# Kernel tuning notes

Measured on AMD Instinct MI355X. Metric: run time of the kernel, lower is better.

## Reference

```python
import jax, jax.numpy as jnp
import numpy as np

E, T, D, N_RBF, N_SBF = 262144, 1048576, 128, 6, 42


def setup_inputs() -> dict:
    key = jax.random.key(0)
    ks = jax.random.split(key, 24)
    s = 0.05
    inp = {
        "m_ji": jax.random.normal(ks[0], (E, D), jnp.float32),
        "e_rbf": jax.random.normal(ks[1], (E, N_RBF), jnp.float32),
        "a_sbf": jax.random.normal(ks[2], (T, N_SBF), jnp.float32),
        "nbr_list": jax.random.randint(ks[3], (E, 2), 0, 65536),
        "kj_idx": jax.random.randint(ks[4], (T,), 0, E),
        "ji_idx": jax.random.randint(ks[5], (T,), 0, E),
        # edge branch params
        "We": jax.random.normal(ks[6], (N_RBF, D), jnp.float32) * s,
        "W_e1": jax.random.normal(ks[7], (D, D), jnp.float32) * s,
        "b_e1": jnp.zeros((D,), jnp.float32),
        "W_e2": jax.random.normal(ks[8], (D, D), jnp.float32) * s,
        "b_e2": jnp.zeros((D,), jnp.float32),
        "W_e3": jax.random.normal(ks[9], (D, D), jnp.float32) * s,
        "b_e3": jnp.zeros((D,), jnp.float32),
        "W_e4": jax.random.normal(ks[10], (D, D), jnp.float32) * s,
        # angle branch params
        "Wa": jax.random.normal(ks[11], (N_SBF, D), jnp.float32) * s,
        "W_a1": jax.random.normal(ks[12], (D, D), jnp.float32) * s,
        "b_a1": jnp.zeros((D,), jnp.float32),
        "W_a2": jax.random.normal(ks[13], (D, D), jnp.float32) * s,
        "b_a2": jnp.zeros((D,), jnp.float32),
        "W_a3": jax.random.normal(ks[14], (D, D), jnp.float32) * s,
        "b_a3": jnp.zeros((D,), jnp.float32),
        "W_a4": jax.random.normal(ks[15], (D, D), jnp.float32) * s,
    }
    return inp


def _mlp(x, W1, b1, W2, b2, W3, b3, W4):
    x = jax.nn.silu(x @ W1 + b1)
    x = jax.nn.silu(x @ W2 + b2)
    x = jax.nn.silu(x @ W3 + b3)
    return x @ W4


def reference(m_ji, e_rbf, a_sbf, nbr_list, kj_idx, ji_idx,
              We, W_e1, b_e1, W_e2, b_e2, W_e3, b_e3, W_e4,
              Wa, W_a1, b_a1, W_a2, b_a2, W_a3, b_a3, W_a4):
    # edge branch: project rbf to embed dim, gate by edge messages  [E, D]
    edge_feats = _mlp((e_rbf @ We) * m_ji, W_e1, b_e1, W_e2, b_e2, W_e3, b_e3, W_e4)
    # angle branch: project sbf, gate by triplet-gathered message sum  [T, D]
    angle_gate = m_ji[kj_idx] + m_ji[ji_idx]
    angle_feats = _mlp((a_sbf @ Wa) * angle_gate, W_a1, b_a1, W_a2, b_a2, W_a3, b_a3, W_a4)
    return (edge_feats, angle_feats)
```

## Files before the change

kernel.cpp:

```cpp
#include <hip/hip_runtime.h>
#include <stdint.h>

typedef __attribute__((ext_vector_type(8))) short bf16x8;
typedef __attribute__((ext_vector_type(4))) float f32x4;
typedef __attribute__((ext_vector_type(8))) unsigned short us8;
typedef __bf16 bf16v2 __attribute__((ext_vector_type(2)));

#define T_CNT 1048576
#define E_CNT 262144

static __device__ __forceinline__ unsigned short f2bf_u(float f) {
  __bf16 h = (__bf16)f;
  return __builtin_bit_cast(unsigned short, h);
}
static __device__ __forceinline__ uint32_t pack2bf(float a, float b) {
  bf16v2 t; t[0] = (__bf16)a; t[1] = (__bf16)b;
  return __builtin_bit_cast(uint32_t, t);
}
static __device__ __forceinline__ float silu_f(float v) {
  float e = __builtin_amdgcn_exp2f(v * -1.44269504088896341f);
  return v * __builtin_amdgcn_rcpf(1.0f + e);
}
static __device__ __forceinline__ bf16x8 frag8(f32x4 a, f32x4 b) {
  union { bf16x8 v; uint32_t u[4]; } r;
  r.u[0] = pack2bf(a[0], a[1]); r.u[1] = pack2bf(a[2], a[3]);
  r.u[2] = pack2bf(b[0], b[1]); r.u[3] = pack2bf(b[2], b[3]);
  return r.v;
}

template<bool LAST>
static __device__ __forceinline__ void layer_mfma(
    const char* __restrict__ src, char* __restrict__ dst,
    const char* __restrict__ wbase,
    const float* __restrict__ bias,
    float* __restrict__ gout,
    int l15, int q, int w, int rs)
{
  f32x4 acc[2][4];
  #pragma unroll
  for (int rg = 0; rg < 2; ++rg)
    #pragma unroll
    for (int c = 0; c < 4; ++c) { f32x4 z = {0.f,0.f,0.f,0.f}; acc[rg][c] = z; }

  const int lane16 = (l15 | (q << 4)) * 16;
  #pragma unroll
  for (int ks = 0; ks < 4; ++ks) {
    bf16x8 wf[4];
    #pragma unroll
    for (int c = 0; c < 4; ++c)
      wf[c] = *(const bf16x8*)(wbase + (((w * 4 + c) * 4 + ks) << 10) + lane16);
    bf16x8 xf0 = *(const bf16x8*)(src + ((l15 * 256 + ks * 64 + q * 16) ^ rs));
    bf16x8 xf1 = *(const bf16x8*)(src + (((16 + l15) * 256 + ks * 64 + q * 16) ^ rs));
    #pragma unroll
    for (int c = 0; c < 4; ++c) {
      acc[0][c] = __builtin_amdgcn_mfma_f32_16x16x32_bf16(wf[c], xf0, acc[0][c], 0, 0, 0);
      acc[1][c] = __builtin_amdgcn_mfma_f32_16x16x32_bf16(wf[c], xf1, acc[1][c], 0, 0, 0);
    }
  }

  #pragma unroll
  for (int rg = 0; rg < 2; ++rg) {
    const int row = rg * 16 + l15;
    #pragma unroll
    for (int c = 0; c < 4; ++c) {
      if (!LAST) {
        f32x4 bv = *(const f32x4*)(bias + w * 64 + c * 16 + q * 4);
        uint2 u;
        u.x = pack2bf(silu_f(acc[rg][c][0] + bv[0]), silu_f(acc[rg][c][1] + bv[1]));
        u.y = pack2bf(silu_f(acc[rg][c][2] + bv[2]), silu_f(acc[rg][c][3] + bv[3]));
        *(uint2*)(dst + ((row * 256 + w * 128 + c * 32 + q * 8) ^ rs)) = u;
      } else {
        __builtin_nontemporal_store(acc[rg][c],
            (f32x4*)(gout + (size_t)row * 128 + w * 64 + c * 16 + q * 4));
      }
    }
  }
}

__global__ __launch_bounds__(128)
__attribute__((amdgpu_waves_per_eu(4, 5)))
void angle_kernel(
    const float* __restrict__ m_ji, const float* __restrict__ a_sbf,
    const int* __restrict__ kj, const int* __restrict__ ji,
    const float* __restrict__ b1, const float* __restrict__ b2,
    const float* __restrict__ b3,
    const char* __restrict__ wt4, const char* __restrict__ waT,
    float* __restrict__ out)
{
  __shared__ __align__(16) char xbA[8192];
  __shared__ __align__(16) char xbB[8192];
  const int tid = threadIdx.x, lane = tid & 63, w = tid >> 6;
  const int l15 = lane & 15, q = lane >> 4;
  const int rs = (l15 & 7) << 4;
  const size_t tb = (size_t)blockIdx.x * 32;
  const int lane16 = lane * 16;

  #pragma unroll
  for (int rg = 0; rg < 2; ++rg) {
    const int row = rg * 16 + l15;
    const size_t grow = tb + row;
    const int ikj = kj[grow], iji = ji[grow];
    const float* ap = a_sbf + grow * 42;
    f32x4 a0 = *(const f32x4*)(ap + q * 8);
    f32x4 a1 = *(const f32x4*)(ap + q * 8 + 4);
    f32x4 c0 = {0.f,0.f,0.f,0.f}, c1 = {0.f,0.f,0.f,0.f};
    if (q == 0) { c0 = *(const f32x4*)(ap + 32); c1 = *(const f32x4*)(ap + 36); }
    else if (q == 1) { float2 t = *(const float2*)(ap + 40); c0[0] = t.x; c0[1] = t.y; }
    bf16x8 f0 = frag8(a0, a1);
    bf16x8 f1 = frag8(c0, c1);
    #pragma unroll
    for (int c = 0; c < 4; ++c) {
      const int ct = w * 4 + c;
      bf16x8 wa0 = *(const bf16x8*)(waT + ((ct * 2 + 0) << 10) + lane16);
      bf16x8 wa1 = *(const bf16x8*)(waT + ((ct * 2 + 1) << 10) + lane16);
      f32x4 acc = {0.f,0.f,0.f,0.f};
      acc = __builtin_amdgcn_mfma_f32_16x16x32_bf16(wa0, f0, acc, 0, 0, 0);
      acc = __builtin_amdgcn_mfma_f32_16x16x32_bf16(wa1, f1, acc, 0, 0, 0);
      const float* bk = m_ji + (size_t)ikj * 128 + ct * 16 + q * 4;
      const float* bj = m_ji + (size_t)iji * 128 + ct * 16 + q * 4;
      f32x4 pk = *(const f32x4*)(bk);
      f32x4 pj = *(const f32x4*)(bj);
      f32x4 g = pk + pj;
      uint2 u;
      u.x = pack2bf(acc[0] * g[0], acc[1] * g[1]);
      u.y = pack2bf(acc[2] * g[2], acc[3] * g[3]);
      *(uint2*)(xbA + ((row * 256 + w * 128 + c * 32 + q * 8) ^ rs)) = u;
    }
  }
  __syncthreads();

  layer_mfma<false>(xbA, xbB, wt4,           b1, nullptr, l15, q, w, rs);
  __syncthreads();
  layer_mfma<false>(xbB, xbA, wt4 + 32768,   b2, nullptr, l15, q, w, rs);
  __syncthreads();
  layer_mfma<false>(xbA, xbB, wt4 + 65536,   b3, nullptr, l15, q, w, rs);
  __syncthreads();
  layer_mfma<true >(xbB, nullptr, wt4 + 98304, nullptr,
                    out + tb * 128, l15, q, w, rs);
}

__global__ __launch_bounds__(128)
__attribute__((amdgpu_waves_per_eu(4, 5)))
void edge_kernel(
    const float* __restrict__ m_ji, const float* __restrict__ e_rbf,
    const float* __restrict__ b1, const float* __restrict__ b2,
    const float* __restrict__ b3,
    const char* __restrict__ wt4, const char* __restrict__ weT,
    float* __restrict__ out)
{
  __shared__ __align__(16) char xbA[8192];
  __shared__ __align__(16) char xbB[8192];
  const int tid = threadIdx.x, lane = tid & 63, w = tid >> 6;
  const int l15 = lane & 15, q = lane >> 4;
  const int rs = (l15 & 7) << 4;
  const size_t tb = (size_t)blockIdx.x * 32;
  const int lane16 = lane * 16;

  #pragma unroll
  for (int rg = 0; rg < 2; ++rg) {
    const int row = rg * 16 + l15;
    const size_t grow = tb + row;
    const float* ep = e_rbf + grow * 6;
    f32x4 a0 = {0.f,0.f,0.f,0.f}, a1 = {0.f,0.f,0.f,0.f};
    if (q == 0) {
      a0 = *(const f32x4*)(ep);
      float2 t = *(const float2*)(ep + 4);
      a1[0] = t.x; a1[1] = t.y;
    }
    bf16x8 ef = frag8(a0, a1);
    #pragma unroll
    for (int c = 0; c < 4; ++c) {
      const int ct = w * 4 + c;
      bf16x8 we = *(const bf16x8*)(weT + (ct << 10) + lane16);
      f32x4 acc = {0.f,0.f,0.f,0.f};
      acc = __builtin_amdgcn_mfma_f32_16x16x32_bf16(we, ef, acc, 0, 0, 0);
      f32x4 g = *(const f32x4*)(m_ji + grow * 128 + ct * 16 + q * 4);
      uint2 u;
      u.x = pack2bf(acc[0] * g[0], acc[1] * g[1]);
      u.y = pack2bf(acc[2] * g[2], acc[3] * g[3]);
      *(uint2*)(xbA + ((row * 256 + w * 128 + c * 32 + q * 8) ^ rs)) = u;
    }
  }
  __syncthreads();

  layer_mfma<false>(xbA, xbB, wt4,           b1, nullptr, l15, q, w, rs);
  __syncthreads();
  layer_mfma<false>(xbB, xbA, wt4 + 32768,   b2, nullptr, l15, q, w, rs);
  __syncthreads();
  layer_mfma<false>(xbA, xbB, wt4 + 65536,   b3, nullptr, l15, q, w, rs);
  __syncthreads();
  layer_mfma<true >(xbB, nullptr, wt4 + 98304, nullptr,
                    out + tb * 128, l15, q, w, rs);
}

__global__ void prep_kernel(
    const float* __restrict__ W0, const float* __restrict__ W1,
    const float* __restrict__ W2, const float* __restrict__ W3,
    const float* __restrict__ W4, const float* __restrict__ W5,
    const float* __restrict__ W6, const float* __restrict__ W7,
    const float* __restrict__ Wa, const float* __restrict__ We,
    char* __restrict__ ws)
{
  const int gid = blockIdx.x * 256 + threadIdx.x;
  const int lane = gid & 63;
  const int l15 = lane & 15, q = lane >> 4;
  if (gid < 16384) {
    const int mat = gid >> 11;
    const int ctks = (gid & 2047) >> 6;
    const int n = (ctks >> 2) * 16 + l15;
    const int k0 = (ctks & 3) * 32 + q * 8;
    const float* W;
    switch (mat) {
      case 0: W = W0; break; case 1: W = W1; break;
      case 2: W = W2; break; case 3: W = W3; break;
      case 4: W = W4; break; case 5: W = W5; break;
      case 6: W = W6; break; default: W = W7; break;
    }
    us8 v;
    #pragma unroll
    for (int j = 0; j < 8; ++j) v[j] = f2bf_u(W[(size_t)(k0 + j) * 128 + n]);
    *(us8*)(ws + mat * 32768 + ctks * 1024 + lane * 16) = v;
  } else if (gid < 17408) {
    const int g = gid - 16384;
    const int ctks = g >> 6;
    const int n = (ctks >> 1) * 16 + l15;
    const int k0 = (ctks & 1) * 32 + q * 8;
    us8 v;
    #pragma unroll
    for (int j = 0; j < 8; ++j) {
      const int k = k0 + j;
      v[j] = (k < 42) ? f2bf_u(Wa[(size_t)k * 128 + n]) : (unsigned short)0;
    }
    *(us8*)(ws + 262144 + ctks * 1024 + lane * 16) = v;
  } else if (gid < 17920) {
    const int g = gid - 17408;
    const int ct = g >> 6;
    const int n = ct * 16 + l15;
    const int k0 = q * 8;
    us8 v;
    #pragma unroll
    for (int j = 0; j < 8; ++j) {
      const int k = k0 + j;
      v[j] = (k < 6) ? f2bf_u(We[(size_t)k * 128 + n]) : (unsigned short)0;
    }
    *(us8*)(ws + 278528 + ct * 1024 + lane * 16) = v;
  }
}

extern "C" void kernel_launch(void* const* d_in, const int* in_sizes, int n_in,
                              void* d_out, int out_size, void* d_ws, size_t ws_size,
                              hipStream_t stream) {
  (void)in_sizes; (void)n_in; (void)out_size; (void)ws_size;
  const float* m_ji  = (const float*)d_in[0];
  const float* e_rbf = (const float*)d_in[1];
  const float* a_sbf = (const float*)d_in[2];
  const int*   kj    = (const int*)d_in[4];
  const int*   ji    = (const int*)d_in[5];
  const float* We    = (const float*)d_in[6];
  const float* We1   = (const float*)d_in[7];
  const float* be1   = (const float*)d_in[8];
  const float* We2   = (const float*)d_in[9];
  const float* be2   = (const float*)d_in[10];
  const float* We3   = (const float*)d_in[11];
  const float* be3   = (const float*)d_in[12];
  const float* We4   = (const float*)d_in[13];
  const float* Wa    = (const float*)d_in[14];
  const float* Wa1   = (const float*)d_in[15];
  const float* ba1   = (const float*)d_in[16];
  const float* Wa2   = (const float*)d_in[17];
  const float* ba2   = (const float*)d_in[18];
  const float* Wa3   = (const float*)d_in[19];
  const float* ba3   = (const float*)d_in[20];
  const float* Wa4   = (const float*)d_in[21];
  char* ws = (char*)d_ws;
  float* out = (float*)d_out;

  prep_kernel<<<70, 256, 0, stream>>>(
      We1, We2, We3, We4, Wa1, Wa2, Wa3, Wa4, Wa, We, ws);
  edge_kernel<<<E_CNT / 32, 128, 0, stream>>>(
      m_ji, e_rbf, be1, be2, be3, ws, ws + 278528, out);
  angle_kernel<<<T_CNT / 32, 128, 0, stream>>>(
      m_ji, a_sbf, kj, ji, ba1, ba2, ba3, ws + 131072, ws + 262144,
      out + (size_t)E_CNT * 128);
}
```

Measured before the change: 580.0 us.

## Restructure MLP kernels to 64-row tiles with 4 waves and lean loops

Blocks grow from 32 rows and 2 waves to 64 rows and 4 waves, each wave owning 32 output columns. The four dense layers become a rolled loop that keeps only one accumulator live and reuses each weight fragment across four row groups. The gather of m_ji is hoisted ahead of the sbf/rbf projection. The aim is lower register pressure, higher occupancy and less repeated weight loading, at the cost of more LDS per block, loops that are no longer unrolled, and dependent MFMA chains on a single accumulator.

```diff
diff --git a/kernel.cpp b/kernel.cpp
--- a/kernel.cpp
+++ b/kernel.cpp
@@ -28,58 +28,81 @@
   return r.v;
 }
 
-template<bool LAST>
-static __device__ __forceinline__ void layer_mfma(
-    const char* __restrict__ src, char* __restrict__ dst,
-    const char* __restrict__ wbase,
-    const float* __restrict__ bias,
-    float* __restrict__ gout,
+static __device__ __forceinline__ void mlp4_lean(
+    char* __restrict__ xbA, char* __restrict__ xbB,
+    const char* __restrict__ wt4,
+    const float* __restrict__ b1, const float* __restrict__ b2,
+    const float* __restrict__ b3, float* __restrict__ outT,
     int l15, int q, int w, int rs)
 {
-  f32x4 acc[2][4];
-  #pragma unroll
-  for (int rg = 0; rg < 2; ++rg)
-    #pragma unroll
-    for (int c = 0; c < 4; ++c) { f32x4 z = {0.f,0.f,0.f,0.f}; acc[rg][c] = z; }
-
+  const int cb = w * 32;
   const int lane16 = (l15 | (q << 4)) * 16;
-  #pragma unroll
-  for (int ks = 0; ks < 4; ++ks) {
-    bf16x8 wf[4];
-    #pragma unroll
-    for (int c = 0; c < 4; ++c)
-      wf[c] = *(const bf16x8*)(wbase + (((w * 4 + c) * 4 + ks) << 10) + lane16);
-    bf16x8 xf0 = *(const bf16x8*)(src + ((l15 * 256 + ks * 64 + q * 16) ^ rs));
-    bf16x8 xf1 = *(const bf16x8*)(src + (((16 + l15) * 256 + ks * 64 + q * 16) ^ rs));
-    #pragma unroll
-    for (int c = 0; c < 4; ++c) {
-      acc[0][c] = __builtin_amdgcn_mfma_f32_16x16x32_bf16(wf[c], xf0, acc[0][c], 0, 0, 0);
-      acc[1][c] = __builtin_amdgcn_mfma_f32_16x16x32_bf16(wf[c], xf1, acc[1][c], 0, 0, 0);
-    }
-  }
-
-  #pragma unroll
-  for (int rg = 0; rg < 2; ++rg) {
-    const int row = rg * 16 + l15;
-    #pragma unroll
-    for (int c = 0; c < 4; ++c) {
-      if (!LAST) {
-        f32x4 bv = *(const f32x4*)(bias + w * 64 + c * 16 + q * 4);
+  const char* src = xbA;
+  char* dst = xbB;
+
+  #pragma unroll 1
+  for (int L = 0; L < 3; ++L) {
+    const char* wb = wt4 + (L << 15);
+    const float* bp = (L == 0) ? b1 : (L == 1) ? b2 : b3;
+    #pragma unroll 1
+    for (int ct = 0; ct < 2; ++ct) {
+      const char* wcb = wb + (((w * 2 + ct) * 4) << 10);
+      bf16x8 wf0 = *(const bf16x8*)(wcb + lane16);
+      bf16x8 wf1 = *(const bf16x8*)(wcb + 1024 + lane16);
+      bf16x8 wf2 = *(const bf16x8*)(wcb + 2048 + lane16);
+      bf16x8 wf3 = *(const bf16x8*)(wcb + 3072 + lane16);
+      f32x4 bv = *(const f32x4*)(bp + cb + ct * 16 + q * 4);
+      #pragma unroll
+      for (int rg = 0; rg < 4; ++rg) {
+        const int row = rg * 16 + l15;
+        bf16x8 xf0 = *(const bf16x8*)(src + ((row * 256 + q * 16) ^ rs));
+        bf16x8 xf1 = *(const bf16x8*)(src + ((row * 256 + 64 + q * 16) ^ rs));
+        bf16x8 xf2 = *(const bf16x8*)(src + ((row * 256 + 128 + q * 16) ^ rs));
+        bf16x8 xf3 = *(const bf16x8*)(src + ((row * 256 + 192 + q * 16) ^ rs));
+        f32x4 acc = {0.f,0.f,0.f,0.f};
+        acc = __builtin_amdgcn_mfma_f32_16x16x32_bf16(wf0, xf0, acc, 0, 0, 0);
+        acc = __builtin_amdgcn_mfma_f32_16x16x32_bf16(wf1, xf1, acc, 0, 0, 0);
+        acc = __builtin_amdgcn_mfma_f32_16x16x32_bf16(wf2, xf2, acc, 0, 0, 0);
+        acc = __builtin_amdgcn_mfma_f32_16x16x32_bf16(wf3, xf3, acc, 0, 0, 0);
         uint2 u;
-        u.x = pack2bf(silu_f(acc[rg][c][0] + bv[0]), silu_f(acc[rg][c][1] + bv[1]));
-        u.y = pack2bf(silu_f(acc[rg][c][2] + bv[2]), silu_f(acc[rg][c][3] + bv[3]));
-        *(uint2*)(dst + ((row * 256 + w * 128 + c * 32 + q * 8) ^ rs)) = u;
-      } else {
-        __builtin_nontemporal_store(acc[rg][c],
-            (f32x4*)(gout + (size_t)row * 128 + w * 64 + c * 16 + q * 4));
+        u.x = pack2bf(silu_f(acc[0] + bv[0]), silu_f(acc[1] + bv[1]));
+        u.y = pack2bf(silu_f(acc[2] + bv[2]), silu_f(acc[3] + bv[3]));
+        *(uint2*)(dst + ((row * 256 + cb * 2 + ct * 32 + q * 8) ^ rs)) = u;
       }
     }
-  }
-}
-
-__global__ __launch_bounds__(128)
-__attribute__((amdgpu_waves_per_eu(4, 5)))
-void angle_kernel(
+    __syncthreads();
+    const char* t = src; src = dst; dst = (char*)t;
+  }
+
+  {
+    const char* wb = wt4 + (3 << 15);
+    #pragma unroll 1
+    for (int ct = 0; ct < 2; ++ct) {
+      const char* wcb = wb + (((w * 2 + ct) * 4) << 10);
+      bf16x8 wf0 = *(const bf16x8*)(wcb + lane16);
+      bf16x8 wf1 = *(const bf16x8*)(wcb + 1024 + lane16);
+      bf16x8 wf2 = *(const bf16x8*)(wcb + 2048 + lane16);
+      bf16x8 wf3 = *(const bf16x8*)(wcb + 3072 + lane16);
+      #pragma unroll
+      for (int rg = 0; rg < 4; ++rg) {
+        const int row = rg * 16 + l15;
+        bf16x8 xf0 = *(const bf16x8*)(src + ((row * 256 + q * 16) ^ rs));
+        bf16x8 xf1 = *(const bf16x8*)(src + ((row * 256 + 64 + q * 16) ^ rs));
+        bf16x8 xf2 = *(const bf16x8*)(src + ((row * 256 + 128 + q * 16) ^ rs));
+        bf16x8 xf3 = *(const bf16x8*)(src + ((row * 256 + 192 + q * 16) ^ rs));
+        f32x4 acc = {0.f,0.f,0.f,0.f};
+        acc = __builtin_amdgcn_mfma_f32_16x16x32_bf16(wf0, xf0, acc, 0, 0, 0);
+        acc = __builtin_amdgcn_mfma_f32_16x16x32_bf16(wf1, xf1, acc, 0, 0, 0);
+        acc = __builtin_amdgcn_mfma_f32_16x16x32_bf16(wf2, xf2, acc, 0, 0, 0);
+        acc = __builtin_amdgcn_mfma_f32_16x16x32_bf16(wf3, xf3, acc, 0, 0, 0);
+        __builtin_nontemporal_store(acc,
+            (f32x4*)(outT + (size_t)row * 128 + cb + ct * 16 + q * 4));
+      }
+    }
+  }
+}
+
+__global__ __launch_bounds__(256) void angle_kernel(
     const float* __restrict__ m_ji, const float* __restrict__ a_sbf,
     const int* __restrict__ kj, const int* __restrict__ ji,
     const float* __restrict__ b1, const float* __restrict__ b2,
@@ -87,19 +110,31 @@
     const char* __restrict__ wt4, const char* __restrict__ waT,
     float* __restrict__ out)
 {
-  __shared__ __align__(16) char xbA[8192];
-  __shared__ __align__(16) char xbB[8192];
+  __shared__ __align__(16) char xbA[16384];
+  __shared__ __align__(16) char xbB[16384];
   const int tid = threadIdx.x, lane = tid & 63, w = tid >> 6;
   const int l15 = lane & 15, q = lane >> 4;
   const int rs = (l15 & 7) << 4;
-  const size_t tb = (size_t)blockIdx.x * 32;
-  const int lane16 = lane * 16;
-
-  #pragma unroll
-  for (int rg = 0; rg < 2; ++rg) {
+  const size_t tb = (size_t)blockIdx.x * 64;
+  const int cb = w * 32;
+
+  bf16x8 wa00 = *(const bf16x8*)(waT + (((w * 2 + 0) * 2 + 0) << 10) + lane * 16);
+  bf16x8 wa01 = *(const bf16x8*)(waT + (((w * 2 + 0) * 2 + 1) << 10) + lane * 16);
+  bf16x8 wa10 = *(const bf16x8*)(waT + (((w * 2 + 1) * 2 + 0) << 10) + lane * 16);
+  bf16x8 wa11 = *(const bf16x8*)(waT + (((w * 2 + 1) * 2 + 1) << 10) + lane * 16);
+
+  #pragma unroll 1
+  for (int rg = 0; rg < 4; ++rg) {
     const int row = rg * 16 + l15;
     const size_t grow = tb + row;
     const int ikj = kj[grow], iji = ji[grow];
+    const float* bk = m_ji + (size_t)ikj * 128 + cb + q * 4;
+    const float* bj = m_ji + (size_t)iji * 128 + cb + q * 4;
+    f32x4 pk0 = *(const f32x4*)(bk);
+    f32x4 pk1 = *(const f32x4*)(bk + 16);
+    f32x4 pj0 = *(const f32x4*)(bj);
+    f32x4 pj1 = *(const f32x4*)(bj + 16);
+
     const float* ap = a_sbf + grow * 42;
     f32x4 a0 = *(const f32x4*)(ap + q * 8);
     f32x4 a1 = *(const f32x4*)(ap + q * 8 + 4);
@@ -108,58 +143,54 @@
     else if (q == 1) { float2 t = *(const float2*)(ap + 40); c0[0] = t.x; c0[1] = t.y; }
     bf16x8 f0 = frag8(a0, a1);
     bf16x8 f1 = frag8(c0, c1);
-    #pragma unroll
-    for (int c = 0; c < 4; ++c) {
-      const int ct = w * 4 + c;
-      bf16x8 wa0 = *(const bf16x8*)(waT + ((ct * 2 + 0) << 10) + lane16);
-      bf16x8 wa1 = *(const bf16x8*)(waT + ((ct * 2 + 1) << 10) + lane16);
-      f32x4 acc = {0.f,0.f,0.f,0.f};
-      acc = __builtin_amdgcn_mfma_f32_16x16x32_bf16(wa0, f0, acc, 0, 0, 0);
-      acc = __builtin_amdgcn_mfma_f32_16x16x32_bf16(wa1, f1, acc, 0, 0, 0);
-      const float* bk = m_ji + (size_t)ikj * 128 + ct * 16 + q * 4;
-      const float* bj = m_ji + (size_t)iji * 128 + ct * 16 + q * 4;
-      f32x4 pk = *(const f32x4*)(bk);
-      f32x4 pj = *(const f32x4*)(bj);
-      f32x4 g = pk + pj;
-      uint2 u;
-      u.x = pack2bf(acc[0] * g[0], acc[1] * g[1]);
-      u.y = pack2bf(acc[2] * g[2], acc[3] * g[3]);
-      *(uint2*)(xbA + ((row * 256 + w * 128 + c * 32 + q * 8) ^ rs)) = u;
-    }
+
+    f32x4 acc0 = {0.f,0.f,0.f,0.f}, acc1 = {0.f,0.f,0.f,0.f};
+    acc0 = __builtin_amdgcn_mfma_f32_16x16x32_bf16(wa00, f0, acc0, 0, 0, 0);
+    acc0 = __builtin_amdgcn_mfma_f32_16x16x32_bf16(wa01, f1, acc0, 0, 0, 0);
+    acc1 = __builtin_amdgcn_mfma_f32_16x16x32_bf16(wa10, f0, acc1, 0, 0, 0);
+    acc1 = __builtin_amdgcn_mfma_f32_16x16x32_bf16(wa11, f1, acc1, 0, 0, 0);
+
+    f32x4 g0 = pk0 + pj0;
+    f32x4 g1 = pk1 + pj1;
+    uint2 u0, u1;
+    u0.x = pack2bf(acc0[0] * g0[0], acc0[1] * g0[1]);
+    u0.y = pack2bf(acc0[2] * g0[2], acc0[3] * g0[3]);
+    u1.x = pack2bf(acc1[0] * g1[0], acc1[1] * g1[1]);
+    u1.y = pack2bf(acc1[2] * g1[2], acc1[3] * g1[3]);
+    *(uint2*)(xbA + ((row * 256 + cb * 2 + q * 8) ^ rs)) = u0;
+    *(uint2*)(xbA + ((row * 256 + cb * 2 + 32 + q * 8) ^ rs)) = u1;
   }
   __syncthreads();
 
-  layer_mfma<false>(xbA, xbB, wt4,           b1, nullptr, l15, q, w, rs);
-  __syncthreads();
-  layer_mfma<false>(xbB, xbA, wt4 + 32768,   b2, nullptr, l15, q, w, rs);
-  __syncthreads();
-  layer_mfma<false>(xbA, xbB, wt4 + 65536,   b3, nullptr, l15, q, w, rs);
-  __syncthreads();
-  layer_mfma<true >(xbB, nullptr, wt4 + 98304, nullptr,
-                    out + tb * 128, l15, q, w, rs);
-}
-
-__global__ __launch_bounds__(128)
-__attribute__((amdgpu_waves_per_eu(4, 5)))
-void edge_kernel(
+  mlp4_lean(xbA, xbB, wt4, b1, b2, b3, out + tb * 128, l15, q, w, rs);
+}
+
+__global__ __launch_bounds__(256) void edge_kernel(
     const float* __restrict__ m_ji, const float* __restrict__ e_rbf,
     const float* __restrict__ b1, const float* __restrict__ b2,
     const float* __restrict__ b3,
     const char* __restrict__ wt4, const char* __restrict__ weT,
     float* __restrict__ out)
 {
-  __shared__ __align__(16) char xbA[8192];
-  __shared__ __align__(16) char xbB[8192];
+  __shared__ __align__(16) char xbA[16384];
+  __shared__ __align__(16) char xbB[16384];
   const int tid = threadIdx.x, lane = tid & 63, w = tid >> 6;
   const int l15 = lane & 15, q = lane >> 4;
   const int rs = (l15 & 7) << 4;
-  const size_t tb = (size_t)blockIdx.x * 32;
-  const int lane16 = lane * 16;
-
-  #pragma unroll
-  for (int rg = 0; rg < 2; ++rg) {
+  const size_t tb = (size_t)blockIdx.x * 64;
+  const int cb = w * 32;
+
+  bf16x8 we0 = *(const bf16x8*)(weT + ((w * 2 + 0) << 10) + lane * 16);
+  bf16x8 we1 = *(const bf16x8*)(weT + ((w * 2 + 1) << 10) + lane * 16);
+
+  #pragma unroll 1
+  for (int rg = 0; rg < 4; ++rg) {
     const int row = rg * 16 + l15;
     const size_t grow = tb + row;
+    const float* bm = m_ji + grow * 128 + cb + q * 4;
+    f32x4 m0 = *(const f32x4*)(bm);
+    f32x4 m1 = *(const f32x4*)(bm + 16);
+
     const float* ep = e_rbf + grow * 6;
     f32x4 a0 = {0.f,0.f,0.f,0.f}, a1 = {0.f,0.f,0.f,0.f};
     if (q == 0) {
@@ -168,29 +199,22 @@
       a1[0] = t.x; a1[1] = t.y;
     }
     bf16x8 ef = frag8(a0, a1);
-    #pragma unroll
-    for (int c = 0; c < 4; ++c) {
-      const int ct = w * 4 + c;
-      bf16x8 we = *(const bf16x8*)(weT + (ct << 10) + lane16);
-      f32x4 acc = {0.f,0.f,0.f,0.f};
-      acc = __builtin_amdgcn_mfma_f32_16x16x32_bf16(we, ef, acc, 0, 0, 0);
-      f32x4 g = *(const f32x4*)(m_ji + grow * 128 + ct * 16 + q * 4);
-      uint2 u;
-      u.x = pack2bf(acc[0] * g[0], acc[1] * g[1]);
-      u.y = pack2bf(acc[2] * g[2], acc[3] * g[3]);
-      *(uint2*)(xbA + ((row * 256 + w * 128 + c * 32 + q * 8) ^ rs)) = u;
-    }
+
+    f32x4 acc0 = {0.f,0.f,0.f,0.f}, acc1 = {0.f,0.f,0.f,0.f};
+    acc0 = __builtin_amdgcn_mfma_f32_16x16x32_bf16(we0, ef, acc0, 0, 0, 0);
+    acc1 = __builtin_amdgcn_mfma_f32_16x16x32_bf16(we1, ef, acc1, 0, 0, 0);
+
+    uint2 u0, u1;
+    u0.x = pack2bf(acc0[0] * m0[0], acc0[1] * m0[1]);
+    u0.y = pack2bf(acc0[2] * m0[2], acc0[3] * m0[3]);
+    u1.x = pack2bf(acc1[0] * m1[0], acc1[1] * m1[1]);
+    u1.y = pack2bf(acc1[2] * m1[2], acc1[3] * m1[3]);
+    *(uint2*)(xbA + ((row * 256 + cb * 2 + q * 8) ^ rs)) = u0;
+    *(uint2*)(xbA + ((row * 256 + cb * 2 + 32 + q * 8) ^ rs)) = u1;
   }
   __syncthreads();
 
-  layer_mfma<false>(xbA, xbB, wt4,           b1, nullptr, l15, q, w, rs);
-  __syncthreads();
-  layer_mfma<false>(xbB, xbA, wt4 + 32768,   b2, nullptr, l15, q, w, rs);
-  __syncthreads();
-  layer_mfma<false>(xbA, xbB, wt4 + 65536,   b3, nullptr, l15, q, w, rs);
-  __syncthreads();
-  layer_mfma<true >(xbB, nullptr, wt4 + 98304, nullptr,
-                    out + tb * 128, l15, q, w, rs);
+  mlp4_lean(xbA, xbB, wt4, b1, b2, b3, out + tb * 128, l15, q, w, rs);
 }
 
 __global__ void prep_kernel(
@@ -274,12 +298,12 @@
   const float* Wa4   = (const float*)d_in[21];
   char* ws = (char*)d_ws;
   float* out = (float*)d_out;
+  float* out_a = out + (size_t)E_CNT * 128;
 
   prep_kernel<<<70, 256, 0, stream>>>(
       We1, We2, We3, We4, Wa1, Wa2, Wa3, Wa4, Wa, We, ws);
-  edge_kernel<<<E_CNT / 32, 128, 0, stream>>>(
+  edge_kernel<<<E_CNT / 64, 256, 0, stream>>>(
       m_ji, e_rbf, be1, be2, be3, ws, ws + 278528, out);
-  angle_kernel<<<T_CNT / 32, 128, 0, stream>>>(
-      m_ji, a_sbf, kj, ji, ba1, ba2, ba3, ws + 131072, ws + 262144,
-      out + (size_t)E_CNT * 128);
-}
+  angle_kernel<<<T_CNT / 64, 256, 0, stream>>>(
+      m_ji, a_sbf, kj, ji, ba1, ba2, ba3, ws + 131072, ws + 262144, out_a);
+}
```

New measurement: 623.0 us. 1.07x slower.
